# Kernel tuning notes

Measured on AMD Instinct MI355X. Metric: run time of the kernel, lower is better.

The kernel has to match this reference:

```python
import jax, jax.numpy as jnp
import numpy as np

D = 256; H = 8; DK = D // H
NT, NW, ND = 2000, 50000, 20000
E_TT, E_WT, E_TD, E_WD = 128000, 256000, 320000, 320000
SQRT_DK = float(np.sqrt(DK))


def setup_inputs() -> dict:
    key = jax.random.key(0)
    ks = jax.random.split(key, 32)
    def nrm(i, shape, s=0.05):
        return jax.random.normal(ks[i], shape, jnp.float32) * s
    inp = {
        "feat_topic": nrm(0, (NT, D), 1.0),
        "feat_word": nrm(1, (NW, D), 1.0),
        "feat_doc": nrm(2, (ND, D), 1.0),
        "ht_prev": nrm(3, (NT, D), 1.0),
        # stacked per-ntype linears, index: 0=topic, 1=word, 2=doc
        "Wk": nrm(4, (3, D, D)), "bk": nrm(5, (3, D)),
        "Wq": nrm(6, (3, D, D)), "bq": nrm(7, (3, D)),
        "Wv": nrm(8, (3, D, D)), "bv": nrm(9, (3, D)),
        # a_linears, index: 0=topic, 1=doc
        "Wa": nrm(10, (2, D, D)), "ba": nrm(11, (2, D)),
        "ln_g": jnp.ones((2, D), jnp.float32),
        "ln_b": jnp.zeros((2, D), jnp.float32),
        "skip": jnp.ones((2,), jnp.float32),
        # RNNCell for topic
        "Wih": nrm(12, (D, D)), "Whh": nrm(13, (D, D)),
        "bih": nrm(14, (D,)), "bhh": nrm(15, (D,)),
        # relation params, index: 0=tt, 1=wt, 2=td, 3=wd
        "rel_pri": jnp.ones((4, H), jnp.float32),
        "rel_att": nrm(16, (4, H, DK, DK), 0.1),
        "rel_msg": nrm(17, (4, H, DK, DK), 0.1),
        "src_tt": jax.random.randint(ks[18], (E_TT,), 0, NT),
        "dst_tt": jnp.arange(E_TT, dtype=jnp.int32) % NT,
        "src_wt": jax.random.randint(ks[19], (E_WT,), 0, NW),
        "dst_wt": jnp.arange(E_WT, dtype=jnp.int32) % NT,
        "src_td": jax.random.randint(ks[20], (E_TD,), 0, NT),
        "dst_td": jnp.arange(E_TD, dtype=jnp.int32) % ND,
        "src_wd": jax.random.randint(ks[21], (E_WD,), 0, NW),
        "dst_wd": jnp.arange(E_WD, dtype=jnp.int32) % ND,
    }
    return inp


def _proj(x, W, b):
    return (x @ W + b).reshape(-1, H, DK)


def _layernorm(x, g, b):
    mu = x.mean(-1, keepdims=True)
    var = ((x - mu) ** 2).mean(-1, keepdims=True)
    return (x - mu) * jax.lax.rsqrt(var + 1e-5) * g + b


def _rel_message(k, v, q, src, dst, pri, A_att, A_msg, n_dst):
    # k,v: [N_src,H,DK]; q: [N_dst,H,DK]; per-edge gather-compute-scatter
    key = jnp.einsum('ehd,hdo->eho', k[src], A_att)          # [E,H,DK]
    att = (q[dst] * key).sum(-1) * pri / SQRT_DK             # [E,H]
    val = jnp.einsum('ehd,hdo->eho', v[src], A_msg)          # [E,H,DK]
    m = jax.ops.segment_max(att, dst, num_segments=n_dst)
    e = jnp.exp(att - m[dst])
    s = jax.ops.segment_sum(e, dst, num_segments=n_dst)
    a = e / s[dst]                                           # edge softmax per dst
    t = jax.ops.segment_sum(a[..., None] * val, dst, num_segments=n_dst)
    return jax.nn.relu(t.reshape(n_dst, D))


def reference(feat_topic, feat_word, feat_doc, ht_prev, Wk, bk, Wq, bq, Wv, bv,
              Wa, ba, ln_g, ln_b, skip, Wih, Whh, bih, bhh,
              rel_pri, rel_att, rel_msg,
              src_tt, dst_tt, src_wt, dst_wt, src_td, dst_td, src_wd, dst_wd):
    # ---- phase 1: messages into topic nodes (etypes tt, wt) ----
    k_t = _proj(feat_topic, Wk[0], bk[0]); v_t = _proj(feat_topic, Wv[0], bv[0])
    k_w = _proj(feat_word,  Wk[1], bk[1]); v_w = _proj(feat_word,  Wv[1], bv[1])
    q_t = _proj(feat_topic, Wq[0], bq[0])
    t_tt = _rel_message(k_t, v_t, q_t, src_tt, dst_tt, rel_pri[0], rel_att[0], rel_msg[0], NT)
    t_wt = _rel_message(k_w, v_w, q_t, src_wt, dst_wt, rel_pri[1], rel_att[1], rel_msg[1], NT)
    t_topic = 0.5 * (t_tt + t_wt)                            # cross_reducer='mean'
    alpha = jax.nn.sigmoid(skip[0])
    trans = t_topic @ Wa[0] + ba[0]
    mix = trans * alpha + feat_topic * (1.0 - alpha)
    h = jnp.tanh(mix @ Wih + bih + ht_prev @ Whh + bhh)      # RNNCell
    topic_out = _layernorm(h, ln_g[0], ln_b[0])
    # ---- phase 2: messages into doc nodes (etypes td, wd), topic uses updated feats ----
    k_t2 = _proj(topic_out, Wk[0], bk[0]); v_t2 = _proj(topic_out, Wv[0], bv[0])
    q_d = _proj(feat_doc, Wq[2], bq[2])
    t_td = _rel_message(k_t2, v_t2, q_d, src_td, dst_td, rel_pri[2], rel_att[2], rel_msg[2], ND)
    t_wd = _rel_message(k_w, v_w, q_d, src_wd, dst_wd, rel_pri[3], rel_att[3], rel_msg[3], ND)
    t_doc = 0.5 * (t_td + t_wd)
    alpha2 = jax.nn.sigmoid(skip[1])
    trans2 = t_doc @ Wa[1] + ba[1]
    mix2 = trans2 * alpha2 + feat_doc * (1.0 - alpha2)
    doc_out = _layernorm(mix2, ln_g[1], ln_b[1])
    return topic_out, doc_out
```

## Files before the change

### kernel.cpp

```cpp
#include <hip/hip_runtime.h>
#include <hip/hip_bf16.h>
#include <hip/hip_fp8.h>

typedef __attribute__((ext_vector_type(8))) short bf16x8;
typedef __attribute__((ext_vector_type(4))) float f32x4;
typedef __attribute__((ext_vector_type(2))) float f32x2;

constexpr int NT = 2000, NW = 50000, ND = 20000;
constexpr float INV_SQRT_DK = 0.17677669529663687f;

__device__ inline float bfu(unsigned short u) {
    return __uint_as_float(((unsigned int)u) << 16);
}
__device__ inline float blo(unsigned int u) { return __uint_as_float(u << 16); }
__device__ inline float bhi(unsigned int u) { return __uint_as_float(u & 0xffff0000u); }
__device__ inline short f2bf(float x) {
    __hip_bfloat16 h = __float2bfloat16(x);
    short s; __builtin_memcpy(&s, &h, 2); return s;
}

__device__ inline void dec4(unsigned int w, float* o) {
#if __has_builtin(__builtin_amdgcn_cvt_pk_f32_fp8)
    f32x2 a = __builtin_amdgcn_cvt_pk_f32_fp8(w, false);
    f32x2 b = __builtin_amdgcn_cvt_pk_f32_fp8(w, true);
    o[0] = a[0]; o[1] = a[1]; o[2] = b[0]; o[3] = b[1];
#else
    __hip_fp8_e4m3 t0, t1, t2, t3;
    t0.__x = (__hip_fp8_storage_t)(w & 0xff);
    t1.__x = (__hip_fp8_storage_t)((w >> 8) & 0xff);
    t2.__x = (__hip_fp8_storage_t)((w >> 16) & 0xff);
    t3.__x = (__hip_fp8_storage_t)((w >> 24) & 0xff);
    o[0] = (float)t0; o[1] = (float)t1; o[2] = (float)t2; o[3] = (float)t3;
#endif
}
__device__ inline unsigned char f2fp8(float v) {
#if __has_builtin(__builtin_amdgcn_cvt_pk_fp8_f32)
    return (unsigned char)(__builtin_amdgcn_cvt_pk_fp8_f32(v, v, 0u, false) & 0xff);
#else
    __hip_fp8_e4m3 h(v); return (unsigned char)h.__x;
#endif
}

__device__ inline void cstore(float* p, float v) { *p = v; }
__device__ inline void cstore(short* p, float v) { *p = f2bf(v); }
__device__ inline void cstore(unsigned char* p, float v) { *p = f2fp8(v); }

__device__ inline void cstore4(float* p, float4 v) {
    *reinterpret_cast<float4*>(p) = v;
}
__device__ inline void cstore4(short* p, float4 v) {
    short4 s; s.x = f2bf(v.x); s.y = f2bf(v.y); s.z = f2bf(v.z); s.w = f2bf(v.w);
    *reinterpret_cast<short4*>(p) = s;
}
__device__ inline void cstore4(unsigned char* p, float4 v) {
#if __has_builtin(__builtin_amdgcn_cvt_pk_fp8_f32)
    unsigned int w = __builtin_amdgcn_cvt_pk_fp8_f32(v.x, v.y, 0u, false);
    w = __builtin_amdgcn_cvt_pk_fp8_f32(v.z, v.w, w, true);
    *reinterpret_cast<unsigned int*>(p) = w;
#else
    p[0] = f2fp8(v.x); p[1] = f2fp8(v.y); p[2] = f2fp8(v.z); p[3] = f2fp8(v.w);
#endif
}

__device__ inline void gload16(const short* g, short* l) {
    __builtin_amdgcn_global_load_lds(
        (const __attribute__((address_space(1))) void*)g,
        (__attribute__((address_space(3))) void*)l, 16, 0, 0);
}

__device__ inline float dot32f8(const unsigned char* __restrict__ kp, const float* __restrict__ qh) {
    const uint4 u = *reinterpret_cast<const uint4*>(kp);
    const uint4 v = *reinterpret_cast<const uint4*>(kp + 16);
    const unsigned int ws[8] = {u.x, u.y, u.z, u.w, v.x, v.y, v.z, v.w};
    float d = 0.f;
    #pragma unroll
    for (int c = 0; c < 8; ++c) {
        float f[4];
        dec4(ws[c], f);
        d += qh[c * 4 + 0] * f[0] + qh[c * 4 + 1] * f[1]
           + qh[c * 4 + 2] * f[2] + qh[c * 4 + 3] * f[3];
    }
    return d;
}

__global__ __launch_bounds__(256) void cvt_bf16(
    const float* __restrict__ src, short* __restrict__ dst, int n8)
{
    const int i = blockIdx.x * 256 + threadIdx.x;
    if (i >= n8) return;
    const float* p = src + (long)i * 8;
    const float4 x0 = *reinterpret_cast<const float4*>(p);
    const float4 x1 = *reinterpret_cast<const float4*>(p + 4);
    bf16x8 v;
    v[0] = f2bf(x0.x); v[1] = f2bf(x0.y); v[2] = f2bf(x0.z); v[3] = f2bf(x0.w);
    v[4] = f2bf(x1.x); v[5] = f2bf(x1.y); v[6] = f2bf(x1.z); v[7] = f2bf(x1.w);
    *reinterpret_cast<bf16x8*>(dst + (long)i * 8) = v;
}

__global__ __launch_bounds__(256) void fold_kernel(
    const float* __restrict__ Wk, const float* __restrict__ bk,
    const float* __restrict__ Wv, const float* __restrict__ bv,
    const float* __restrict__ rel_att, const float* __restrict__ rel_msg,
    short* __restrict__ B_t1, short* __restrict__ B_w, short* __restrict__ B_t2,
    float* __restrict__ bias_t1, float* __restrict__ bias_w, float* __restrict__ bias_t2)
{
    const int f = blockIdx.x >> 3, chunk = blockIdx.x & 7;
    const int rel = f >> 1, isV = f & 1;
    const int ntype = (rel == 1 || rel == 3) ? 1 : 0;
    const float* Wsrc = (isV ? Wv : Wk) + ntype * 65536;
    const float* bsrc = (isV ? bv : bk) + ntype * 256;
    const float* A    = (isV ? rel_msg : rel_att) + rel * 8192;
    short* wdst; float* bdst;
    switch (f) {
        case 0: wdst = B_t1 + 65536;     bdst = bias_t1 + 256; break;
        case 1: wdst = B_t1 + 2 * 65536; bdst = bias_t1 + 512; break;
        case 2: wdst = B_w;              bdst = bias_w;        break;
        case 3: wdst = B_w + 65536;      bdst = bias_w + 256;  break;
        case 4: wdst = B_t2;             bdst = bias_t2;       break;
        case 5: wdst = B_t2 + 65536;     bdst = bias_t2 + 256; break;
        case 6: wdst = B_w + 2 * 65536;  bdst = bias_w + 512;  break;
        default: wdst = B_w + 3 * 65536; bdst = bias_w + 768;  break;
    }
    __shared__ float Wsh[32][256];
    const int tid = threadIdx.x;
    for (int i = 0; i < 32; ++i)
        Wsh[i][tid] = Wsrc[(chunk * 32 + i) * 256 + tid];
    __syncthreads();
    const int h = tid >> 5, o = tid & 31;
    float a[32];
    #pragma unroll
    for (int d = 0; d < 32; ++d) a[d] = A[h * 1024 + d * 32 + o];
    short tmp[32];
    #pragma unroll
    for (int r = 0; r < 32; ++r) {
        float s = 0.f;
        #pragma unroll
        for (int d = 0; d < 32; ++d) s = fmaf(Wsh[r][(h << 5) + d], a[d], s);
        tmp[r] = f2bf(s);
    }
    short* wp = wdst + tid * 256 + chunk * 32;
    #pragma unroll
    for (int r8 = 0; r8 < 4; ++r8) {
        bf16x8 v;
        #pragma unroll
        for (int t = 0; t < 8; ++t) v[t] = tmp[r8 * 8 + t];
        *reinterpret_cast<bf16x8*>(wp + r8 * 8) = v;
    }
    if (chunk == 0) {
        float s = 0.f;
        #pragma unroll
        for (int d = 0; d < 32; ++d) s = fmaf(bsrc[(h << 5) + d], a[d], s);
        bdst[tid] = s;
    }
}

struct TransP { const float* s[6]; short* d[6]; };
__global__ __launch_bounds__(256) void wtrans6(TransP p) {
    const int m = blockIdx.y, n = blockIdx.x, k = threadIdx.x;
    p.d[m][n * 256 + k] = f2bf(p.s[m][k * 256 + n]);
}

__global__ void copy_bias(const float* __restrict__ s, float* __restrict__ d) {
    d[threadIdx.x] = s[threadIdx.x];
}

template <typename OutT, int EPI, int NI>
__device__ inline void epilogue(
    f32x4 (&acc)[NI][4], const float* __restrict__ bias, OutT* __restrict__ C,
    int M, int ldc, const float* __restrict__ extra,
    const float* __restrict__ skipv, int skipIdx,
    int row0, int col0, int wm, int wn, int r, int kb)
{
    float alpha = 0.f;
    if (EPI == 1) alpha = 1.f / (1.f + __expf(-skipv[skipIdx]));
    float4 b4[4];
    #pragma unroll
    for (int j = 0; j < 4; ++j)
        b4[j] = *reinterpret_cast<const float4*>(&bias[col0 + wn * 64 + j * 16 + kb * 4]);
    #pragma unroll
    for (int i = 0; i < NI; ++i) {
        const int rrow = row0 + wm * 64 + i * 16 + r;
        if (rrow >= M) continue;
        #pragma unroll
        for (int j = 0; j < 4; ++j) {
            const int cb = col0 + wn * 64 + j * 16 + kb * 4;
            float4 v;
            v.x = acc[i][j][0] + b4[j].x;
            v.y = acc[i][j][1] + b4[j].y;
            v.z = acc[i][j][2] + b4[j].z;
            v.w = acc[i][j][3] + b4[j].w;
            if (EPI == 1) {
                const float4 e = *reinterpret_cast<const float4*>(&extra[rrow * 256 + cb]);
                v.x = alpha * v.x + (1.f - alpha) * e.x;
                v.y = alpha * v.y + (1.f - alpha) * e.y;
                v.z = alpha * v.z + (1.f - alpha) * e.z;
                v.w = alpha * v.w + (1.f - alpha) * e.w;
            }
            if (EPI == 2) {
                const float4 e = *reinterpret_cast<const float4*>(&extra[rrow * 256 + cb]);
                v.x = tanhf(v.x + e.x);
                v.y = tanhf(v.y + e.y);
                v.z = tanhf(v.z + e.z);
                v.w = tanhf(v.w + e.w);
            }
            cstore4(C + rrow * ldc + cb, v);
        }
    }
}

template <bool XF32, typename OutT, int EPI, bool SWZ>
__global__ __launch_bounds__(256) void gemm_lds(
    const void* __restrict__ Xv, const short* __restrict__ Wt,
    const float* __restrict__ bias, OutT* __restrict__ C,
    int M, int ldc, const float* __restrict__ extra,
    const float* __restrict__ skipv, int skipIdx)
{
    __shared__ short As[128 * 64];
    __shared__ short Bs[128 * 64];
    int bxi = blockIdx.x, byi = blockIdx.y;
    if constexpr (SWZ) {
        const int h = bxi + (int)gridDim.x * byi;
        const int i = h >> 3;
        byi = (h & 7) + 8 * (i >> 3);
        bxi = i & 7;
        if (byi * 128 >= M) return;
    }
    const int tid = threadIdx.x;
    const int wave = tid >> 6, lane = tid & 63;
    const int wm = wave >> 1, wn = wave & 1;
    const int r = lane & 15, kb = lane >> 4;
    const int col0 = bxi * 128;
    const int row0 = byi * 128;

    const int l8 = lane >> 3;
    const int c8 = lane & 7;
    const int swz8 = c8 ^ l8;
    f32x4 acc[4][4] = {};

    for (int k0 = 0; k0 < 256; k0 += 64) {
        if (k0) __syncthreads();
        if constexpr (XF32) {
            #pragma unroll
            for (int q = 0; q < 4; ++q) {
                const int rl = wave * 32 + q * 8 + l8;
                const int grow = min(row0 + rl, M - 1);
                const float* xp = (const float*)Xv + grow * 256 + k0 + c8 * 8;
                const float4 x0 = *reinterpret_cast<const float4*>(xp);
                const float4 x1 = *reinterpret_cast<const float4*>(xp + 4);
                bf16x8 v;
                v[0] = f2bf(x0.x); v[1] = f2bf(x0.y); v[2] = f2bf(x0.z); v[3] = f2bf(x0.w);
                v[4] = f2bf(x1.x); v[5] = f2bf(x1.y); v[6] = f2bf(x1.z); v[7] = f2bf(x1.w);
                *reinterpret_cast<bf16x8*>(As + rl * 64 + swz8 * 8) = v;
            }
        } else {
            #pragma unroll
            for (int q = 0; q < 4; ++q) {
                const int rl = wave * 32 + q * 8 + l8;
                const int grow = min(row0 + rl, M - 1);
                gload16((const short*)Xv + grow * 256 + k0 + swz8 * 8,
                        As + (wave * 32 + q * 8) * 64);
            }
        }
        #pragma unroll
        for (int q = 0; q < 4; ++q) {
            const int cl = wave * 32 + q * 8 + l8;
            gload16(Wt + (col0 + cl) * 256 + k0 + swz8 * 8,
                    Bs + (wave * 32 + q * 8) * 64);
        }
        __syncthreads();
        #pragma unroll
        for (int s = 0; s < 2; ++s) {
            const int csw = ((kb + 4 * s) ^ (r & 7)) * 8;
            bf16x8 af[4], bw[4];
            #pragma unroll
            for (int i = 0; i < 4; ++i) {
                af[i] = *reinterpret_cast<const bf16x8*>(As + (wm * 64 + i * 16 + r) * 64 + csw);
                bw[i] = *reinterpret_cast<const bf16x8*>(Bs + (wn * 64 + i * 16 + r) * 64 + csw);
            }
            #pragma unroll
            for (int i = 0; i < 4; ++i)
                #pragma unroll
                for (int j = 0; j < 4; ++j)
                    acc[i][j] = __builtin_amdgcn_mfma_f32_16x16x32_bf16(bw[j], af[i], acc[i][j], 0, 0, 0);
        }
    }
    epilogue<OutT, EPI, 4>(acc, bias, C, M, ldc, extra, skipv, skipIdx,
                           row0, col0, wm, wn, r, kb);
}

__global__ __launch_bounds__(256) void gemm_qkv(
    const float* __restrict__ X, const short* __restrict__ Wt,
    const float* __restrict__ bias, short* __restrict__ Qo,
    unsigned char* __restrict__ KVo, int M,
    const float* __restrict__ X2, const short* __restrict__ Wt2,
    const float* __restrict__ bias2, float* __restrict__ Ro)
{
    __shared__ short As[128 * 64];
    __shared__ short Bs[128 * 64];
    const int bxi = blockIdx.x, byi = blockIdx.y;
    const bool isR = bxi >= 6;
    const float* Xp = isR ? X2 : X;
    const short* Wp = isR ? Wt2 : Wt;
    const float* bp = isR ? bias2 : bias;
    const int colW = isR ? (bxi - 6) * 128 : bxi * 128;
    const int tid = threadIdx.x;
    const int wave = tid >> 6, lane = tid & 63;
    const int wm = wave >> 1, wn = wave & 1;
    const int r = lane & 15, kb = lane >> 4;
    const int row0 = byi * 128;

    const int l8 = lane >> 3;
    const int c8 = lane & 7;
    const int swz8 = c8 ^ l8;
    f32x4 acc[4][4] = {};

    for (int k0 = 0; k0 < 256; k0 += 64) {
        if (k0) __syncthreads();
        #pragma unroll
        for (int q = 0; q < 4; ++q) {
            const int rl = wave * 32 + q * 8 + l8;
            const int grow = min(row0 + rl, M - 1);
            const float* xp = Xp + grow * 256 + k0 + c8 * 8;
            const float4 x0 = *reinterpret_cast<const float4*>(xp);
            const float4 x1 = *reinterpret_cast<const float4*>(xp + 4);
            bf16x8 v;
            v[0] = f2bf(x0.x); v[1] = f2bf(x0.y); v[2] = f2bf(x0.z); v[3] = f2bf(x0.w);
            v[4] = f2bf(x1.x); v[5] = f2bf(x1.y); v[6] = f2bf(x1.z); v[7] = f2bf(x1.w);
            *reinterpret_cast<bf16x8*>(As + rl * 64 + swz8 * 8) = v;
        }
        #pragma unroll
        for (int q = 0; q < 4; ++q) {
            const int cl = wave * 32 + q * 8 + l8;
            gload16(Wp + (colW + cl) * 256 + k0 + swz8 * 8,
                    Bs + (wave * 32 + q * 8) * 64);
        }
        __syncthreads();
        #pragma unroll
        for (int s = 0; s < 2; ++s) {
            const int csw = ((kb + 4 * s) ^ (r & 7)) * 8;
            bf16x8 af[4], bw[4];
            #pragma unroll
            for (int i = 0; i < 4; ++i) {
                af[i] = *reinterpret_cast<const bf16x8*>(As + (wm * 64 + i * 16 + r) * 64 + csw);
                bw[i] = *reinterpret_cast<const bf16x8*>(Bs + (wn * 64 + i * 16 + r) * 64 + csw);
            }
            #pragma unroll
            for (int i = 0; i < 4; ++i)
                #pragma unroll
                for (int j = 0; j < 4; ++j)
                    acc[i][j] = __builtin_amdgcn_mfma_f32_16x16x32_bf16(bw[j], af[i], acc[i][j], 0, 0, 0);
        }
    }

    float4 b4[4];
    #pragma unroll
    for (int j = 0; j < 4; ++j)
        b4[j] = *reinterpret_cast<const float4*>(&bp[colW + wn * 64 + j * 16 + kb * 4]);
    #pragma unroll
    for (int i = 0; i < 4; ++i) {
        const int rrow = row0 + wm * 64 + i * 16 + r;
        if (rrow >= M) continue;
        #pragma unroll
        for (int j = 0; j < 4; ++j) {
            const int cb = colW + wn * 64 + j * 16 + kb * 4;
            float4 v;
            v.x = acc[i][j][0] + b4[j].x;
            v.y = acc[i][j][1] + b4[j].y;
            v.z = acc[i][j][2] + b4[j].z;
            v.w = acc[i][j][3] + b4[j].w;
            if (isR)          cstore4(Ro + rrow * 256 + cb, v);
            else if (bxi < 2) cstore4(Qo + rrow * 256 + cb, v);
            else              cstore4(KVo + rrow * 512 + (cb - 256), v);
        }
    }
}

template <bool XF32, typename OutT, int EPI, bool SWZ, bool SWAP>
__global__ __launch_bounds__(512) void gemm_w(
    const void* __restrict__ Xv, const short* __restrict__ Wt,
    const float* __restrict__ bias, OutT* __restrict__ C,
    int M, int ldc, const float* __restrict__ extra,
    const float* __restrict__ skipv, int skipIdx)
{
    __shared__ short As[256 * 64];
    __shared__ short Bs[128 * 64];
    int bxi = blockIdx.x, byi = blockIdx.y;
    if constexpr (SWZ) {
        const int h = bxi + (int)gridDim.x * byi;
        const int i = h >> 3;
        byi = (h & 7) + 8 * (i >> 3);
        bxi = i & 7;
        if (byi * 256 >= M) return;
    }
    const int tid = threadIdx.x;
    const int wave = tid >> 6, lane = tid & 63;
    const int wm = wave >> 1, wn = wave & 1;
    const int r = lane & 15, kb = lane >> 4;
    const int col0 = bxi * 128;
    const int row0 = byi * 256;

    const int l8 = lane >> 3;
    const int c8 = lane & 7;
    const int swz8 = c8 ^ l8;
    f32x4 acc[4][4] = {};

    for (int k0 = 0; k0 < 256; k0 += 64) {
        if (k0) __syncthreads();
        if constexpr (XF32) {
            #pragma unroll
            for (int q = 0; q < 4; ++q) {
                const int rl = wave * 32 + q * 8 + l8;
                const int grow = min(row0 + rl, M - 1);
                const float* xp = (const float*)Xv + grow * 256 + k0 + c8 * 8;
                const float4 x0 = *reinterpret_cast<const float4*>(xp);
                const float4 x1 = *reinterpret_cast<const float4*>(xp + 4);
                bf16x8 v;
                v[0] = f2bf(x0.x); v[1] = f2bf(x0.y); v[2] = f2bf(x0.z); v[3] = f2bf(x0.w);
                v[4] = f2bf(x1.x); v[5] = f2bf(x1.y); v[6] = f2bf(x1.z); v[7] = f2bf(x1.w);
                *reinterpret_cast<bf16x8*>(As + rl * 64 + swz8 * 8) = v;
            }
        } else {
            #pragma unroll
            for (int q = 0; q < 4; ++q) {
                const int rl = wave * 32 + q * 8 + l8;
                const int grow = min(row0 + rl, M - 1);
                gload16((const short*)Xv + grow * 256 + k0 + swz8 * 8,
                        As + (wave * 32 + q * 8) * 64);
            }
        }
        #pragma unroll
        for (int q = 0; q < 2; ++q) {
            const int cl = wave * 16 + q * 8 + l8;
            gload16(Wt + (col0 + cl) * 256 + k0 + swz8 * 8,
                    Bs + (wave * 16 + q * 8) * 64);
        }
        __syncthreads();
        #pragma unroll
        for (int s = 0; s < 2; ++s) {
            const int csw = ((kb + 4 * s) ^ (r & 7)) * 8;
            bf16x8 af[4], bw[4];
            #pragma unroll
            for (int i = 0; i < 4; ++i) {
                af[i] = *reinterpret_cast<const bf16x8*>(As + (wm * 64 + i * 16 + r) * 64 + csw);
                bw[i] = *reinterpret_cast<const bf16x8*>(Bs + (wn * 64 + i * 16 + r) * 64 + csw);
            }
            #pragma unroll
            for (int i = 0; i < 4; ++i)
                #pragma unroll
                for (int j = 0; j < 4; ++j) {
                    if constexpr (SWAP)
                        acc[i][j] = __builtin_amdgcn_mfma_f32_16x16x32_bf16(bw[j], af[i], acc[i][j], 0, 0, 0);
                    else
                        acc[i][j] = __builtin_amdgcn_mfma_f32_16x16x32_bf16(af[i], bw[j], acc[i][j], 0, 0, 0);
                }
        }
    }

    if constexpr (SWAP) {
        epilogue<OutT, EPI, 4>(acc, bias, C, M, ldc, extra, skipv, skipIdx,
                               row0, col0, wm, wn, r, kb);
    } else {
        float alpha = 0.f;
        if (EPI == 1) alpha = 1.f / (1.f + __expf(-skipv[skipIdx]));
        #pragma unroll
        for (int i = 0; i < 4; ++i) {
            #pragma unroll
            for (int j = 0; j < 4; ++j) {
                const int col = col0 + wn * 64 + j * 16 + r;
                const float bc = bias[col];
                #pragma unroll
                for (int t = 0; t < 4; ++t) {
                    const int rrow = row0 + wm * 64 + i * 16 + kb * 4 + t;
                    if (rrow < M) {
                        float v = acc[i][j][t] + bc;
                        if (EPI == 1) v = alpha * v + (1.f - alpha) * extra[rrow * 256 + col];
                        if (EPI == 2) v = tanhf(v + extra[rrow * 256 + col]);
                        cstore(C + rrow * ldc + col, v);
                    }
                }
            }
        }
    }
}

template <int NE>
__device__ inline void rel_scores_f8(const unsigned char* __restrict__ kv, int ld, int koff,
                                     const int* __restrict__ sidx, int off, float scale,
                                     const float* __restrict__ qh, float* __restrict__ sc,
                                     int g, int l)
{
    constexpr int NL = NE / 32;
    float att[NL];
    #pragma unroll
    for (int t = 0; t < NL; ++t)
        att[t] = dot32f8(kv + (size_t)sidx[off + l + 32 * t] * ld + koff + g * 32, qh) * scale;
    float m = att[0];
    #pragma unroll
    for (int t = 1; t < NL; ++t) m = fmaxf(m, att[t]);
    #pragma unroll
    for (int o = 16; o > 0; o >>= 1) m = fmaxf(m, __shfl_xor(m, o));
    float ex[NL], s = 0.f;
    #pragma unroll
    for (int t = 0; t < NL; ++t) { ex[t] = __expf(att[t] - m); s += ex[t]; }
    #pragma unroll
    for (int o = 16; o > 0; o >>= 1) s += __shfl_xor(s, o);
    const float inv = 1.f / s;
    #pragma unroll
    for (int t = 0; t < NL; ++t) sc[(off + l + 32 * t) * 9 + g] = ex[t] * inv;
}

template <int NEA, int NEB>
__global__ __launch_bounds__(256) void msg_k(
    const short* __restrict__ q, int ldq,
    const unsigned char* __restrict__ kvA, int ldA, int koffA, int voffA,
    const int* __restrict__ srcA,
    const unsigned char* __restrict__ kvB, int ldB, int koffB, int voffB,
    const int* __restrict__ srcB,
    const float* __restrict__ relPri, int relA, int relB,
    short* __restrict__ out, int n_dst)
{
    constexpr int NET = NEA + NEB;
    const int j = blockIdx.x, tid = threadIdx.x;
    __shared__ float qsh[256];
    __shared__ int sidx[NET];
    __shared__ float sc[NET * 9];
    __shared__ float ps[8][544];

    if (tid < 64) {
        const ushort4 u = *reinterpret_cast<const ushort4*>(
            (const unsigned short*)q + j * ldq + tid * 4);
        float4 f; f.x = bfu(u.x); f.y = bfu(u.y); f.z = bfu(u.z); f.w = bfu(u.w);
        *reinterpret_cast<float4*>(qsh + tid * 4) = f;
    }
    if (tid < NEA) sidx[tid] = srcA[j + tid * n_dst];
    else if (tid < NET) sidx[tid] = srcB[j + (tid - NEA) * n_dst];
    __syncthreads();

    const int g = tid >> 5, l = tid & 31;
    float qr[32];
    #pragma unroll
    for (int c = 0; c < 8; ++c) {
        const float4 v = *reinterpret_cast<const float4*>(qsh + g * 32 + c * 4);
        qr[c * 4] = v.x; qr[c * 4 + 1] = v.y; qr[c * 4 + 2] = v.z; qr[c * 4 + 3] = v.w;
    }

    if constexpr (NEA == 16 && NEB == 16) {
        const int isB = l >> 4;
        const unsigned char* base = isB ? kvB + koffB : kvA + koffA;
        const int ld = isB ? ldB : ldA;
        const float scale = relPri[(isB ? relB : relA) * 8 + g] * INV_SQRT_DK;
        const float att = dot32f8(base + (size_t)sidx[l] * ld + g * 32, qr) * scale;
        float m = att;
        #pragma unroll
        for (int o = 8; o > 0; o >>= 1) m = fmaxf(m, __shfl_xor(m, o));
        const float ex = __expf(att - m);
        float s = ex;
        #pragma unroll
        for (int o = 8; o > 0; o >>= 1) s += __shfl_xor(s, o);
        sc[l * 9 + g] = ex / s;
    } else {
        rel_scores_f8<NEA>(kvA, ldA, koffA, sidx, 0,
                           relPri[relA * 8 + g] * INV_SQRT_DK, qr, sc, g, l);
        rel_scores_f8<NEB>(kvB, ldB, koffB, sidx, NEA,
                           relPri[relB * 8 + g] * INV_SQRT_DK, qr, sc, g, l);
    }
    __syncthreads();

    const int ct16 = tid & 15;
    const int rel  = (tid >> 4) & 1;
    const int es   = tid >> 5;
    const int hh   = ct16 >> 1;
    const unsigned char* kvR = rel ? kvB : kvA;
    const int ldR   = rel ? ldB : ldA;
    const int voffR = rel ? voffB : voffA;
    const int offR  = rel ? NEA : 0;
    const int neR   = rel ? NEB : NEA;
    float acc[16] = {};
    for (int e = es; e < neR; e += 8) {
        const float w = sc[(offR + e) * 9 + hh];
        const uint4 u = *reinterpret_cast<const uint4*>(
            kvR + (size_t)sidx[offR + e] * ldR + voffR + ct16 * 16);
        float f[16];
        dec4(u.x, f); dec4(u.y, f + 4); dec4(u.z, f + 8); dec4(u.w, f + 12);
        #pragma unroll
        for (int k = 0; k < 16; ++k) acc[k] = fmaf(w, f[k], acc[k]);
    }
    {
        float* pp = &ps[es][rel * 272 + ct16 * 17];
        #pragma unroll
        for (int k = 0; k < 16; ++k) pp[k] = acc[k];
    }
    __syncthreads();

    const int ra = (tid >> 4) * 17 + (tid & 15);
    float rA = 0.f, rB = 0.f;
    #pragma unroll
    for (int e2 = 0; e2 < 8; ++e2) { rA += ps[e2][ra]; rB += ps[e2][272 + ra]; }
    const float val = 0.5f * (fmaxf(rA, 0.f) + fmaxf(rB, 0.f));
    unsigned short* ob = (unsigned short*)qsh;
    ob[tid] = (unsigned short)f2bf(val);
    __syncthreads();
    if (tid < 32) {
        const uint4 u = *reinterpret_cast<const uint4*>(ob + tid * 8);
        *reinterpret_cast<uint4*>((unsigned short*)out + j * 256 + tid * 8) = u;
    }
}

template <bool WB>
__global__ __launch_bounds__(256) void ln_k(
    float* __restrict__ data, const float* __restrict__ g,
    const float* __restrict__ b, int nrows, short* __restrict__ bfout)
{
    const int wid = threadIdx.x >> 6, lane = threadIdx.x & 63;
    const int row = blockIdx.x * 4 + wid;
    if (row >= nrows) return;
    float4 x = *reinterpret_cast<float4*>(data + row * 256 + lane * 4);
    float s  = x.x + x.y + x.z + x.w;
    float q2 = x.x * x.x + x.y * x.y + x.z * x.z + x.w * x.w;
    #pragma unroll
    for (int o = 32; o > 0; o >>= 1) { s += __shfl_xor(s, o); q2 += __shfl_xor(q2, o); }
    const float mu  = s * (1.f / 256.f);
    const float var = q2 * (1.f / 256.f) - mu * mu;
    const float rr = rsqrtf(var + 1e-5f);
    const float4 gg = *reinterpret_cast<const float4*>(g + lane * 4);
    const float4 bb = *reinterpret_cast<const float4*>(b + lane * 4);
    x.x = (x.x - mu) * rr * gg.x + bb.x;
    x.y = (x.y - mu) * rr * gg.y + bb.y;
    x.z = (x.z - mu) * rr * gg.z + bb.z;
    x.w = (x.w - mu) * rr * gg.w + bb.w;
    *reinterpret_cast<float4*>(data + row * 256 + lane * 4) = x;
    if (WB) {
        ushort4 u;
        u.x = (unsigned short)f2bf(x.x); u.y = (unsigned short)f2bf(x.y);
        u.z = (unsigned short)f2bf(x.z); u.w = (unsigned short)f2bf(x.w);
        *reinterpret_cast<ushort4*>((unsigned short*)bfout + row * 256 + lane * 4) = u;
    }
}

extern "C" void kernel_launch(void* const* d_in, const int* in_sizes, int n_in,
                              void* d_out, int out_size, void* d_ws, size_t ws_size,
                              hipStream_t stream)
{
    const float* feat_topic = (const float*)d_in[0];
    const float* feat_word  = (const float*)d_in[1];
    const float* feat_doc   = (const float*)d_in[2];
    const float* ht_prev    = (const float*)d_in[3];
    const float* Wk  = (const float*)d_in[4];
    const float* bk  = (const float*)d_in[5];
    const float* Wq  = (const float*)d_in[6];
    const float* bq  = (const float*)d_in[7];
    const float* Wv  = (const float*)d_in[8];
    const float* bv  = (const float*)d_in[9];
    const float* Wa  = (const float*)d_in[10];
    const float* ba  = (const float*)d_in[11];
    const float* ln_g = (const float*)d_in[12];
    const float* ln_b = (const float*)d_in[13];
    const float* skip = (const float*)d_in[14];
    const float* Wih  = (const float*)d_in[15];
    const float* Whh  = (const float*)d_in[16];
    const float* bih  = (const float*)d_in[17];
    const float* bhh  = (const float*)d_in[18];
    const float* rel_pri = (const float*)d_in[19];
    const float* rel_att = (const float*)d_in[20];
    const float* rel_msg = (const float*)d_in[21];
    const int* src_tt = (const int*)d_in[22];
    const int* src_wt = (const int*)d_in[24];
    const int* src_td = (const int*)d_in[26];
    const int* src_wd = (const int*)d_in[28];

    short* B_t1 = (short*)d_ws;
    short* B_w  = B_t1 + 196608;
    short* B_t2 = B_w + 262144;
    short* Wq2t = B_t2 + 131072;
    short* Whht = Wq2t + 65536;
    short* Wa0t = Whht + 65536;
    short* Wiht = Wa0t + 65536;
    short* Wa1t = Wiht + 65536;
    short* q_t  = Wa1t + 65536;
    unsigned char* kv1 = (unsigned char*)(q_t + 512000);
    unsigned char* w8  = kv1 + 1024000;
    unsigned char* kv2 = w8 + 51200000;
    short* qd   = (short*)(kv2 + 1024000);
    short* ttop = qd + 5120000;
    short* mixb = ttop + 512000;
    short* tdoc = mixb + 512000;
    short* xt2  = tdoc + 5120000;
    float* bias_t1 = (float*)(xt2 + 512000);
    float* bias_w  = bias_t1 + 768;
    float* bias_t2 = bias_w + 1024;
    float* r2      = bias_t2 + 512;
    short* wfb     = (short*)(r2 + 512000);

    float* out_topic = (float*)d_out;
    float* out_doc   = out_topic + NT * 256;

    cvt_bf16<<<dim3(6400), 256, 0, stream>>>(feat_word, wfb, NW * 256 / 8);
    fold_kernel<<<dim3(64), 256, 0, stream>>>(Wk, bk, Wv, bv, rel_att, rel_msg,
                                              B_t1, B_w, B_t2, bias_t1, bias_w, bias_t2);
    TransP tp;
    tp.s[0] = Wq;            tp.d[0] = B_t1;
    tp.s[1] = Wq + 131072;   tp.d[1] = Wq2t;
    tp.s[2] = Whh;           tp.d[2] = Whht;
    tp.s[3] = Wih;           tp.d[3] = Wiht;
    tp.s[4] = Wa;            tp.d[4] = Wa0t;
    tp.s[5] = Wa + 65536;    tp.d[5] = Wa1t;
    wtrans6<<<dim3(256, 6), 256, 0, stream>>>(tp);
    copy_bias<<<dim3(1), 256, 0, stream>>>(bq, bias_t1);

    gemm_w<false, unsigned char, 0, true, false><<<dim3(8, 200), 512, 0, stream>>>(
        wfb, B_w, bias_w, w8, NW, 1024, nullptr, nullptr, 0);

    gemm_qkv<<<dim3(8, 16), 256, 0, stream>>>(
        feat_topic, B_t1, bias_t1, q_t, kv1, NT, ht_prev, Whht, bhh, r2);
    gemm_w<true, short, 0, false, true><<<dim3(2, 79), 512, 0, stream>>>(
        feat_doc, Wq2t, bq + 512, qd, ND, 256, nullptr, nullptr, 0);

    msg_k<64, 128><<<dim3(NT), 256, 0, stream>>>(
        q_t, 256,
        kv1, 512, 0, 256, src_tt,
        w8, 1024, 0, 256, src_wt,
        rel_pri, 0, 1, ttop, NT);

    gemm_lds<false, short, 1, false><<<dim3(2, 16), 256, 0, stream>>>(
        ttop, Wa0t, ba, mixb, NT, 256, feat_topic, skip, 0);
    gemm_lds<false, float, 2, false><<<dim3(2, 16), 256, 0, stream>>>(
        mixb, Wiht, bih, out_topic, NT, 256, r2, nullptr, 0);
    ln_k<true><<<dim3(500), 256, 0, stream>>>(out_topic, ln_g, ln_b, NT, xt2);

    gemm_lds<false, unsigned char, 0, false><<<dim3(4, 16), 256, 0, stream>>>(
        xt2, B_t2, bias_t2, kv2, NT, 512, nullptr, nullptr, 0);

    msg_k<16, 16><<<dim3(ND), 256, 0, stream>>>(
        qd, 256,
        kv2, 512, 0, 256, src_td,
        w8, 1024, 512, 768, src_wd,
        rel_pri, 2, 3, tdoc, ND);

    gemm_w<false, float, 1, false, true><<<dim3(2, 79), 512, 0, stream>>>(
        tdoc, Wa1t, ba + 256, out_doc, ND, 256, feat_doc, skip, 1);
    ln_k<false><<<dim3(5000), 256, 0, stream>>>(out_doc, ln_g + 256, ln_b + 256, ND, nullptr);
}
```

Measured before the change: 252.0 us.

## Store V projections in fp16 with split K/V buffers and half2 accumulation

Keys stay fp8 but values are now written as fp16 into separate K and V buffers, and a dedicated word GEMM writes them in a transposed-store layout. The message kernel accumulates weighted values with packed half2 FMAs instead of decoding fp8 to float, and it reduces per-relation partials through swizzled shared memory. The aim is to cut fp8-decode ALU work in the gather loop and raise value precision. In exchange the V gather traffic doubles, accumulating in fp16 risks precision loss, and the word GEMM epilogue now issues scalar, poorly coalesced stores.

```diff
diff --git a/kernel.cpp b/kernel.cpp
--- a/kernel.cpp
+++ b/kernel.cpp
@@ -1,5 +1,6 @@
 #include <hip/hip_runtime.h>
 #include <hip/hip_bf16.h>
+#include <hip/hip_fp16.h>
 #include <hip/hip_fp8.h>
 
 typedef __attribute__((ext_vector_type(8))) short bf16x8;
@@ -12,8 +13,6 @@
 __device__ inline float bfu(unsigned short u) {
     return __uint_as_float(((unsigned int)u) << 16);
 }
-__device__ inline float blo(unsigned int u) { return __uint_as_float(u << 16); }
-__device__ inline float bhi(unsigned int u) { return __uint_as_float(u & 0xffff0000u); }
 __device__ inline short f2bf(float x) {
     __hip_bfloat16 h = __float2bfloat16(x);
     short s; __builtin_memcpy(&s, &h, 2); return s;
@@ -44,6 +43,7 @@
 __device__ inline void cstore(float* p, float v) { *p = v; }
 __device__ inline void cstore(short* p, float v) { *p = f2bf(v); }
 __device__ inline void cstore(unsigned char* p, float v) { *p = f2fp8(v); }
+__device__ inline void cstore(__half* p, float v) { *p = __float2half(v); }
 
 __device__ inline void cstore4(float* p, float4 v) {
     *reinterpret_cast<float4*>(p) = v;
@@ -60,6 +60,14 @@
 #else
     p[0] = f2fp8(v.x); p[1] = f2fp8(v.y); p[2] = f2fp8(v.z); p[3] = f2fp8(v.w);
 #endif
+}
+__device__ inline void cstore4(__half* p, float4 v) {
+    __half2 a = __floats2half2_rn(v.x, v.y);
+    __half2 b = __floats2half2_rn(v.z, v.w);
+    unsigned int wa, wb;
+    __builtin_memcpy(&wa, &a, 4); __builtin_memcpy(&wb, &b, 4);
+    uint2 u; u.x = wa; u.y = wb;
+    *reinterpret_cast<uint2*>(p) = u;
 }
 
 __device__ inline void gload16(const short* g, short* l) {
@@ -208,7 +216,7 @@
     }
 }
 
-template <bool XF32, typename OutT, int EPI, bool SWZ>
+template <bool XF32, typename OutT, int EPI>
 __global__ __launch_bounds__(256) void gemm_lds(
     const void* __restrict__ Xv, const short* __restrict__ Wt,
     const float* __restrict__ bias, OutT* __restrict__ C,
@@ -217,14 +225,7 @@
 {
     __shared__ short As[128 * 64];
     __shared__ short Bs[128 * 64];
-    int bxi = blockIdx.x, byi = blockIdx.y;
-    if constexpr (SWZ) {
-        const int h = bxi + (int)gridDim.x * byi;
-        const int i = h >> 3;
-        byi = (h & 7) + 8 * (i >> 3);
-        bxi = i & 7;
-        if (byi * 128 >= M) return;
-    }
+    const int bxi = blockIdx.x, byi = blockIdx.y;
     const int tid = threadIdx.x;
     const int wave = tid >> 6, lane = tid & 63;
     const int wm = wave >> 1, wn = wave & 1;
@@ -291,7 +292,7 @@
 __global__ __launch_bounds__(256) void gemm_qkv(
     const float* __restrict__ X, const short* __restrict__ Wt,
     const float* __restrict__ bias, short* __restrict__ Qo,
-    unsigned char* __restrict__ KVo, int M,
+    unsigned char* __restrict__ Ko, __half* __restrict__ Vo, int M,
     const float* __restrict__ X2, const short* __restrict__ Wt2,
     const float* __restrict__ bias2, float* __restrict__ Ro)
 {
@@ -370,7 +371,83 @@
             v.w = acc[i][j][3] + b4[j].w;
             if (isR)          cstore4(Ro + rrow * 256 + cb, v);
             else if (bxi < 2) cstore4(Qo + rrow * 256 + cb, v);
-            else              cstore4(KVo + rrow * 512 + (cb - 256), v);
+            else if (bxi < 4) cstore4(Ko + rrow * 256 + (cb - 256), v);
+            else              cstore4(Vo + rrow * 256 + (cb - 512), v);
+        }
+    }
+}
+
+__global__ __launch_bounds__(256) void gemm_kv2(
+    const short* __restrict__ X, const short* __restrict__ Wt,
+    const float* __restrict__ bias, unsigned char* __restrict__ Ko,
+    __half* __restrict__ Vo, int M)
+{
+    __shared__ short As[128 * 64];
+    __shared__ short Bs[128 * 64];
+    const int bxi = blockIdx.x, byi = blockIdx.y;
+    const int tid = threadIdx.x;
+    const int wave = tid >> 6, lane = tid & 63;
+    const int wm = wave >> 1, wn = wave & 1;
+    const int r = lane & 15, kb = lane >> 4;
+    const int col0 = bxi * 128;
+    const int row0 = byi * 128;
+
+    const int l8 = lane >> 3;
+    const int c8 = lane & 7;
+    const int swz8 = c8 ^ l8;
+    f32x4 acc[4][4] = {};
+
+    for (int k0 = 0; k0 < 256; k0 += 64) {
+        if (k0) __syncthreads();
+        #pragma unroll
+        for (int q = 0; q < 4; ++q) {
+            const int rl = wave * 32 + q * 8 + l8;
+            const int grow = min(row0 + rl, M - 1);
+            gload16(X + grow * 256 + k0 + swz8 * 8,
+                    As + (wave * 32 + q * 8) * 64);
+        }
+        #pragma unroll
+        for (int q = 0; q < 4; ++q) {
+            const int cl = wave * 32 + q * 8 + l8;
+            gload16(Wt + (col0 + cl) * 256 + k0 + swz8 * 8,
+                    Bs + (wave * 32 + q * 8) * 64);
+        }
+        __syncthreads();
+        #pragma unroll
+        for (int s = 0; s < 2; ++s) {
+            const int csw = ((kb + 4 * s) ^ (r & 7)) * 8;
+            bf16x8 af[4], bw[4];
+            #pragma unroll
+            for (int i = 0; i < 4; ++i) {
+                af[i] = *reinterpret_cast<const bf16x8*>(As + (wm * 64 + i * 16 + r) * 64 + csw);
+                bw[i] = *reinterpret_cast<const bf16x8*>(Bs + (wn * 64 + i * 16 + r) * 64 + csw);
+            }
+            #pragma unroll
+            for (int i = 0; i < 4; ++i)
+                #pragma unroll
+                for (int j = 0; j < 4; ++j)
+                    acc[i][j] = __builtin_amdgcn_mfma_f32_16x16x32_bf16(bw[j], af[i], acc[i][j], 0, 0, 0);
+        }
+    }
+
+    float4 b4[4];
+    #pragma unroll
+    for (int j = 0; j < 4; ++j)
+        b4[j] = *reinterpret_cast<const float4*>(&bias[col0 + wn * 64 + j * 16 + kb * 4]);
+    #pragma unroll
+    for (int i = 0; i < 4; ++i) {
+        const int rrow = row0 + wm * 64 + i * 16 + r;
+        if (rrow >= M) continue;
+        #pragma unroll
+        for (int j = 0; j < 4; ++j) {
+            const int cb = col0 + wn * 64 + j * 16 + kb * 4;
+            float4 v;
+            v.x = acc[i][j][0] + b4[j].x;
+            v.y = acc[i][j][1] + b4[j].y;
+            v.z = acc[i][j][2] + b4[j].z;
+            v.w = acc[i][j][3] + b4[j].w;
+            if (bxi < 2) cstore4(Ko + rrow * 256 + cb, v);
+            else         cstore4(Vo + rrow * 256 + (cb - 256), v);
         }
     }
 }
@@ -483,8 +560,91 @@
     }
 }
 
+__global__ __launch_bounds__(512) void gemm_word(
+    const short* __restrict__ Xv, const short* __restrict__ Wt,
+    const float* __restrict__ bias, unsigned char* __restrict__ K8,
+    __half* __restrict__ V16, int M)
+{
+    __shared__ short As[256 * 64];
+    __shared__ short Bs[128 * 64];
+    int bxi = blockIdx.x, byi = blockIdx.y;
+    {
+        const int h = bxi + (int)gridDim.x * byi;
+        const int i = h >> 3;
+        byi = (h & 7) + 8 * (i >> 3);
+        bxi = i & 7;
+        if (byi * 256 >= M) return;
+    }
+    const int tid = threadIdx.x;
+    const int wave = tid >> 6, lane = tid & 63;
+    const int wm = wave >> 1, wn = wave & 1;
+    const int r = lane & 15, kb = lane >> 4;
+    const int col0 = bxi * 128;
+    const int row0 = byi * 256;
+
+    const int l8 = lane >> 3;
+    const int c8 = lane & 7;
+    const int swz8 = c8 ^ l8;
+    f32x4 acc[4][4] = {};
+
+    for (int k0 = 0; k0 < 256; k0 += 64) {
+        if (k0) __syncthreads();
+        #pragma unroll
+        for (int q = 0; q < 4; ++q) {
+            const int rl = wave * 32 + q * 8 + l8;
+            const int grow = min(row0 + rl, M - 1);
+            gload16(Xv + grow * 256 + k0 + swz8 * 8,
+                    As + (wave * 32 + q * 8) * 64);
+        }
+        #pragma unroll
+        for (int q = 0; q < 2; ++q) {
+            const int cl = wave * 16 + q * 8 + l8;
+            gload16(Wt + (col0 + cl) * 256 + k0 + swz8 * 8,
+                    Bs + (wave * 16 + q * 8) * 64);
+        }
+        __syncthreads();
+        #pragma unroll
+        for (int s = 0; s < 2; ++s) {
+            const int csw = ((kb + 4 * s) ^ (r & 7)) * 8;
+            bf16x8 af[4], bw[4];
+            #pragma unroll
+            for (int i = 0; i < 4; ++i) {
+                af[i] = *reinterpret_cast<const bf16x8*>(As + (wm * 64 + i * 16 + r) * 64 + csw);
+                bw[i] = *reinterpret_cast<const bf16x8*>(Bs + (wn * 64 + i * 16 + r) * 64 + csw);
+            }
+            #pragma unroll
+            for (int i = 0; i < 4; ++i)
+                #pragma unroll
+                for (int j = 0; j < 4; ++j)
+                    acc[i][j] = __builtin_amdgcn_mfma_f32_16x16x32_bf16(af[i], bw[j], acc[i][j], 0, 0, 0);
+        }
+    }
+
+    const int seg = bxi >> 1;
+    const bool isV = seg & 1;
+    const int half = seg >> 1;
+    #pragma unroll
+    for (int i = 0; i < 4; ++i) {
+        #pragma unroll
+        for (int j = 0; j < 4; ++j) {
+            const int col = col0 + wn * 64 + j * 16 + r;
+            const float bc = bias[col];
+            const int dcol = half * 256 + (col & 255);
+            #pragma unroll
+            for (int t = 0; t < 4; ++t) {
+                const int rrow = row0 + wm * 64 + i * 16 + kb * 4 + t;
+                if (rrow < M) {
+                    const float v = acc[i][j][t] + bc;
+                    if (isV) V16[(size_t)rrow * 512 + dcol] = __float2half(v);
+                    else     K8[(size_t)rrow * 512 + dcol] = f2fp8(v);
+                }
+            }
+        }
+    }
+}
+
 template <int NE>
-__device__ inline void rel_scores_f8(const unsigned char* __restrict__ kv, int ld, int koff,
+__device__ inline void rel_scores_f8(const unsigned char* __restrict__ kx, int ld,
                                      const int* __restrict__ sidx, int off, float scale,
                                      const float* __restrict__ qh, float* __restrict__ sc,
                                      int g, int l)
@@ -493,7 +653,7 @@
     float att[NL];
     #pragma unroll
     for (int t = 0; t < NL; ++t)
-        att[t] = dot32f8(kv + (size_t)sidx[off + l + 32 * t] * ld + koff + g * 32, qh) * scale;
+        att[t] = dot32f8(kx + (size_t)sidx[off + l + 32 * t] * ld + g * 32, qh) * scale;
     float m = att[0];
     #pragma unroll
     for (int t = 1; t < NL; ++t) m = fmaxf(m, att[t]);
@@ -507,15 +667,39 @@
     const float inv = 1.f / s;
     #pragma unroll
     for (int t = 0; t < NL; ++t) sc[(off + l + 32 * t) * 9 + g] = ex[t] * inv;
+}
+
+template <int NE>
+__device__ inline void accum_f16(const __half* __restrict__ vx, int ld,
+                                 const int* __restrict__ sidx, int off,
+                                 const float* __restrict__ sc,
+                                 int es, int ct, int h, __half2* __restrict__ acc2)
+{
+    #pragma unroll
+    for (int e = es; e < NE; e += 8) {
+        const float w = sc[(off + e) * 9 + h];
+        const __half2 w2 = __float2half2_rn(w);
+        const uint4 u = *reinterpret_cast<const uint4*>(
+            vx + (size_t)sidx[off + e] * ld + ct * 8);
+        __half2 h0, h1, h2, h3;
+        __builtin_memcpy(&h0, &u.x, 4);
+        __builtin_memcpy(&h1, &u.y, 4);
+        __builtin_memcpy(&h2, &u.z, 4);
+        __builtin_memcpy(&h3, &u.w, 4);
+        acc2[0] = __hfma2(h0, w2, acc2[0]);
+        acc2[1] = __hfma2(h1, w2, acc2[1]);
+        acc2[2] = __hfma2(h2, w2, acc2[2]);
+        acc2[3] = __hfma2(h3, w2, acc2[3]);
+    }
 }
 
 template <int NEA, int NEB>
 __global__ __launch_bounds__(256) void msg_k(
     const short* __restrict__ q, int ldq,
-    const unsigned char* __restrict__ kvA, int ldA, int koffA, int voffA,
-    const int* __restrict__ srcA,
-    const unsigned char* __restrict__ kvB, int ldB, int koffB, int voffB,
-    const int* __restrict__ srcB,
+    const unsigned char* __restrict__ kA, int ldkA,
+    const __half* __restrict__ vA, int ldvA, const int* __restrict__ srcA,
+    const unsigned char* __restrict__ kB, int ldkB,
+    const __half* __restrict__ vB, int ldvB, const int* __restrict__ srcB,
     const float* __restrict__ relPri, int relA, int relB,
     short* __restrict__ out, int n_dst)
 {
@@ -524,7 +708,8 @@
     __shared__ float qsh[256];
     __shared__ int sidx[NET];
     __shared__ float sc[NET * 9];
-    __shared__ float ps[8][544];
+    __shared__ float psA[8][256];
+    __shared__ float psB[8][256];
 
     if (tid < 64) {
         const ushort4 u = *reinterpret_cast<const ushort4*>(
@@ -546,8 +731,8 @@
 
     if constexpr (NEA == 16 && NEB == 16) {
         const int isB = l >> 4;
-        const unsigned char* base = isB ? kvB + koffB : kvA + koffA;
-        const int ld = isB ? ldB : ldA;
+        const unsigned char* base = isB ? kB : kA;
+        const int ld = isB ? ldkB : ldkA;
         const float scale = relPri[(isB ? relB : relA) * 8 + g] * INV_SQRT_DK;
         const float att = dot32f8(base + (size_t)sidx[l] * ld + g * 32, qr) * scale;
         float m = att;
@@ -559,43 +744,32 @@
         for (int o = 8; o > 0; o >>= 1) s += __shfl_xor(s, o);
         sc[l * 9 + g] = ex / s;
     } else {
-        rel_scores_f8<NEA>(kvA, ldA, koffA, sidx, 0,
+        rel_scores_f8<NEA>(kA, ldkA, sidx, 0,
                            relPri[relA * 8 + g] * INV_SQRT_DK, qr, sc, g, l);
-        rel_scores_f8<NEB>(kvB, ldB, koffB, sidx, NEA,
+        rel_scores_f8<NEB>(kB, ldkB, sidx, NEA,
                            relPri[relB * 8 + g] * INV_SQRT_DK, qr, sc, g, l);
     }
     __syncthreads();
 
-    const int ct16 = tid & 15;
-    const int rel  = (tid >> 4) & 1;
-    const int es   = tid >> 5;
-    const int hh   = ct16 >> 1;
-    const unsigned char* kvR = rel ? kvB : kvA;
-    const int ldR   = rel ? ldB : ldA;
-    const int voffR = rel ? voffB : voffA;
-    const int offR  = rel ? NEA : 0;
-    const int neR   = rel ? NEB : NEA;
-    float acc[16] = {};
-    for (int e = es; e < neR; e += 8) {
-        const float w = sc[(offR + e) * 9 + hh];
-        const uint4 u = *reinterpret_cast<const uint4*>(
-            kvR + (size_t)sidx[offR + e] * ldR + voffR + ct16 * 16);
-        float f[16];
-        dec4(u.x, f); dec4(u.y, f + 4); dec4(u.z, f + 8); dec4(u.w, f + 12);
-        #pragma unroll
-        for (int k = 0; k < 16; ++k) acc[k] = fmaf(w, f[k], acc[k]);
-    }
-    {
-        float* pp = &ps[es][rel * 272 + ct16 * 17];
-        #pragma unroll
-        for (int k = 0; k < 16; ++k) pp[k] = acc[k];
-    }
+    const int es = tid >> 5, ct = tid & 31, hh = ct >> 2;
+    __half2 accA[4] = {}, accB[4] = {};
+    accum_f16<NEA>(vA, ldvA, sidx, 0,   sc, es, ct, hh, accA);
+    accum_f16<NEB>(vB, ldvB, sidx, NEA, sc, es, ct, hh, accB);
+    const int sw = ct & 4;
+    float2 a0 = __half22float2(accA[0]), a1 = __half22float2(accA[1]);
+    float2 a2 = __half22float2(accA[2]), a3 = __half22float2(accA[3]);
+    float2 b0 = __half22float2(accB[0]), b1 = __half22float2(accB[1]);
+    float2 b2 = __half22float2(accB[2]), b3 = __half22float2(accB[3]);
+    *reinterpret_cast<float4*>(&psA[es][(ct * 8) ^ sw])     = make_float4(a0.x, a0.y, a1.x, a1.y);
+    *reinterpret_cast<float4*>(&psA[es][(ct * 8 + 4) ^ sw]) = make_float4(a2.x, a2.y, a3.x, a3.y);
+    *reinterpret_cast<float4*>(&psB[es][(ct * 8) ^ sw])     = make_float4(b0.x, b0.y, b1.x, b1.y);
+    *reinterpret_cast<float4*>(&psB[es][(ct * 8 + 4) ^ sw]) = make_float4(b2.x, b2.y, b3.x, b3.y);
     __syncthreads();
 
-    const int ra = (tid >> 4) * 17 + (tid & 15);
     float rA = 0.f, rB = 0.f;
-    #pragma unroll
-    for (int e2 = 0; e2 < 8; ++e2) { rA += ps[e2][ra]; rB += ps[e2][272 + ra]; }
+    const int rp = tid ^ ((tid >> 3) & 4);
+    #pragma unroll
+    for (int e2 = 0; e2 < 8; ++e2) { rA += psA[e2][rp]; rB += psB[e2][rp]; }
     const float val = 0.5f * (fmaxf(rA, 0.f) + fmaxf(rB, 0.f));
     unsigned short* ob = (unsigned short*)qsh;
     ob[tid] = (unsigned short)f2bf(val);
@@ -677,19 +851,23 @@
     short* Wiht = Wa0t + 65536;
     short* Wa1t = Wiht + 65536;
     short* q_t  = Wa1t + 65536;
-    unsigned char* kv1 = (unsigned char*)(q_t + 512000);
-    unsigned char* w8  = kv1 + 1024000;
-    unsigned char* kv2 = w8 + 51200000;
-    short* qd   = (short*)(kv2 + 1024000);
+    unsigned char* k_tt = (unsigned char*)(q_t + 512000);
+    __half* v_tt = (__half*)(k_tt + 512000);
+    unsigned char* K8w = (unsigned char*)(v_tt + 512000);
+    __half* V16w = (__half*)(K8w + 25600000);
+    unsigned char* k_td = (unsigned char*)(V16w + 25600000);
+    __half* v_td = (__half*)(k_td + 512000);
+    short* scratch = (short*)(v_td + 512000);
+    short* wfb  = scratch;
+    short* qd   = scratch;
     short* ttop = qd + 5120000;
     short* mixb = ttop + 512000;
     short* tdoc = mixb + 512000;
     short* xt2  = tdoc + 5120000;
-    float* bias_t1 = (float*)(xt2 + 512000);
+    float* bias_t1 = (float*)(scratch + 12800000);
     float* bias_w  = bias_t1 + 768;
     float* bias_t2 = bias_w + 1024;
     float* r2      = bias_t2 + 512;
-    short* wfb     = (short*)(r2 + 512000);
 
     float* out_topic = (float*)d_out;
     float* out_doc   = out_topic + NT * 256;
@@ -707,33 +885,33 @@
     wtrans6<<<dim3(256, 6), 256, 0, stream>>>(tp);
     copy_bias<<<dim3(1), 256, 0, stream>>>(bq, bias_t1);
 
-    gemm_w<false, unsigned char, 0, true, false><<<dim3(8, 200), 512, 0, stream>>>(
-        wfb, B_w, bias_w, w8, NW, 1024, nullptr, nullptr, 0);
+    gemm_word<<<dim3(8, 200), 512, 0, stream>>>(
+        wfb, B_w, bias_w, K8w, V16w, NW);
 
     gemm_qkv<<<dim3(8, 16), 256, 0, stream>>>(
-        feat_topic, B_t1, bias_t1, q_t, kv1, NT, ht_prev, Whht, bhh, r2);
+        feat_topic, B_t1, bias_t1, q_t, k_tt, v_tt, NT, ht_prev, Whht, bhh, r2);
     gemm_w<true, short, 0, false, true><<<dim3(2, 79), 512, 0, stream>>>(
         feat_doc, Wq2t, bq + 512, qd, ND, 256, nullptr, nullptr, 0);
 
     msg_k<64, 128><<<dim3(NT), 256, 0, stream>>>(
         q_t, 256,
-        kv1, 512, 0, 256, src_tt,
-        w8, 1024, 0, 256, src_wt,
+        k_tt, 256, v_tt, 256, src_tt,
+        K8w, 512, V16w, 512, src_wt,
         rel_pri, 0, 1, ttop, NT);
 
-    gemm_lds<false, short, 1, false><<<dim3(2, 16), 256, 0, stream>>>(
+    gemm_lds<false, short, 1><<<dim3(2, 16), 256, 0, stream>>>(
         ttop, Wa0t, ba, mixb, NT, 256, feat_topic, skip, 0);
-    gemm_lds<false, float, 2, false><<<dim3(2, 16), 256, 0, stream>>>(
+    gemm_lds<false, float, 2><<<dim3(2, 16), 256, 0, stream>>>(
         mixb, Wiht, bih, out_topic, NT, 256, r2, nullptr, 0);
     ln_k<true><<<dim3(500), 256, 0, stream>>>(out_topic, ln_g, ln_b, NT, xt2);
 
-    gemm_lds<false, unsigned char, 0, false><<<dim3(4, 16), 256, 0, stream>>>(
-        xt2, B_t2, bias_t2, kv2, NT, 512, nullptr, nullptr, 0);
+    gemm_kv2<<<dim3(4, 16), 256, 0, stream>>>(
+        xt2, B_t2, bias_t2, k_td, v_td, NT);
 
     msg_k<16, 16><<<dim3(ND), 256, 0, stream>>>(
         qd, 256,
-        kv2, 512, 0, 256, src_td,
-        w8, 1024, 512, 768, src_wd,
+        k_td, 256, v_td, 256, src_td,
+        K8w + 256, 512, V16w + 256, 512, src_wd,
         rel_pri, 2, 3, tdoc, ND);
 
     gemm_w<false, float, 1, false, true><<<dim3(2, 79), 512, 0, stream>>>(
```

New measurement: 270.4 us. +7.3%, slower.
